# Optimization experiments

Measured on AMD Instinct MI355X. Metric: run time of the kernel, lower is better.

Reference implementation:

```python
import jax, jax.numpy as jnp
import numpy as np

B, LQ, LK, D = 32, 2048, 2048, 64


def setup_inputs() -> dict:
    key = jax.random.key(0)
    k1, k2, k3, k4 = jax.random.split(key, 4)
    querys = jax.random.normal(k1, (B, LQ, D), dtype=jnp.float32)
    keys = jax.random.normal(k2, (B, LK, D), dtype=jnp.float32)
    values = jax.random.normal(k3, (B, LK, D), dtype=jnp.float32)
    # valid lengths in [1, LK]
    valid_lens = jax.random.randint(k4, (B,), 1, LK + 1, dtype=jnp.int32)
    return {"querys": querys, "keys": keys, "values": values, "valid_lens": valid_lens}


def reference(querys, keys, values, valid_lens):
    d = querys.shape[-1]
    # [B, Lq, Lk] score matrix
    scores = jnp.einsum("bqd,bkd->bqk", querys, keys) / jnp.sqrt(jnp.asarray(d, querys.dtype))
    # masked softmax: key positions >= valid_len get -1e6 (as in d2l masked_softmax)
    key_pos = jnp.arange(scores.shape[-1], dtype=jnp.int32)  # [Lk]
    mask = key_pos[None, None, :] < valid_lens[:, None, None]  # [B, 1, Lk]
    scores = jnp.where(mask, scores, jnp.asarray(-1e6, scores.dtype))
    attn = jax.nn.softmax(scores, axis=-1)
    # dropout p=0.0 -> identity
    return jnp.einsum("bqk,bkd->bqd", attn, values)
```

## Files before the change

kernel.cpp:

```cpp
#include <hip/hip_runtime.h>
#include <hip/hip_bf16.h>
#include <math.h>


#define B_    32
#define LQ_   2048
#define LK_   2048
#define D_    64

typedef __attribute__((ext_vector_type(8)))  short bf16x8;
typedef __attribute__((ext_vector_type(4)))  float f32x4;
typedef __attribute__((ext_vector_type(16))) float f32x16;
typedef __attribute__((ext_vector_type(2)))  unsigned u32x2;

static __device__ __forceinline__ unsigned pk_bf16(float a, float b) {
    __hip_bfloat162 h = __float22bfloat162_rn(float2{a, b});
    return *(unsigned*)&h;
}

static __device__ __forceinline__ u32x2 plswap(unsigned a, unsigned b) {
    return __builtin_amdgcn_permlane32_swap(a, b, false, false);
}
static __device__ __forceinline__ float xhalf_max(float x) {
    u32x2 r = plswap(__float_as_uint(x), __float_as_uint(x));
    return fmaxf(__uint_as_float(r[0]), __uint_as_float(r[1]));
}
static __device__ __forceinline__ float xhalf_add(float x) {
    u32x2 r = plswap(__float_as_uint(x), __float_as_uint(x));
    return __uint_as_float(r[0]) + __uint_as_float(r[1]);
}

template<int NS>
__global__ __launch_bounds__(256, 2) void fa_split6_kernel(
    const float* __restrict__ Q, const float* __restrict__ K,
    const float* __restrict__ V, const int* __restrict__ vlen,
    float* __restrict__ OP, float* __restrict__ ML)
{
    __shared__ __align__(16) short Kl[2][64 * 64];
    __shared__ __align__(16) short Vt[2][64 * 64];
    __shared__ int s_b;

    const int tid  = threadIdx.x;
    const int wid  = tid >> 6;
    const int lane = tid & 63;
    const int c31  = lane & 31;
    const int h    = lane >> 5;

    constexpr int PB = 16 * NS;
    const int L    = blockIdx.x;
    const int rank = L / PB;
    const int sub  = L % PB;
    const int qb   = sub & 15;
    const int s    = sub >> 4;
    if (tid < 32) {
        const int vj = vlen[tid];
        int r = 0;
        for (int k = 0; k < 32; ++k) {
            const int vk = vlen[k];
            r += (vk > vj) || (vk == vj && k < tid);
        }
        if (r == rank) s_b = tid;
    }
    __syncthreads();
    const int b  = s_b;
    const int q0 = qb * 128 + wid * 32;
    const int vl = vlen[b];
    const int nt    = (vl + 63) >> 6;
    const int chunk = (nt + NS - 1) / NS;
    const int t0    = s * chunk;
    const int t1    = min(t0 + chunk, nt);

    const float qscale = 0.125f * 1.44269504088896340736f;

    unsigned qfrag[4][4];
#pragma unroll
    for (int ks = 0; ks < 4; ++ks) {
        const float* qp = Q + ((size_t)(b * LQ_ + q0 + c31)) * D_ + ks * 16 + h * 8;
        f32x4 t0v = *(const f32x4*)qp;
        f32x4 t1v = *(const f32x4*)(qp + 4);
#pragma unroll
        for (int jj = 0; jj < 2; ++jj) {
            qfrag[ks][jj]     = pk_bf16(t0v[2*jj] * qscale, t0v[2*jj+1] * qscale);
            qfrag[ks][jj + 2] = pk_bf16(t1v[2*jj] * qscale, t1v[2*jj+1] * qscale);
        }
    }

    f32x16 oacc[2];
#pragma unroll
    for (int dt = 0; dt < 2; ++dt)
#pragma unroll
        for (int r = 0; r < 16; ++r) oacc[dt][r] = 0.f;
    float mrun = -INFINITY, lrun = 0.f;

    const int skey = tid >> 2, skh = tid & 3;
    const int vkg = tid >> 4, vdg = tid & 15;

    const float* kgp = K + ((size_t)(b * LK_ + skey)) * D_ + skh * 16;
    const float* vgp = V + ((size_t)(b * LK_ + vkg * 4)) * D_ + vdg * 4;

    f32x4 kr[4], vr[4];
    if (t0 < t1) {
        const size_t off = (size_t)t0 * 64 * D_;
#pragma unroll
        for (int i = 0; i < 4; ++i) kr[i] = *(const f32x4*)(kgp + off + 4 * i);
#pragma unroll
        for (int i = 0; i < 4; ++i) vr[i] = *(const f32x4*)(vgp + off + (size_t)i * D_);
    }

    for (int t = t0; t < t1; ++t) {
        const int k0 = t * 64;
        const int buf = t & 1;

        {
            unsigned pk32[8];
#pragma unroll
            for (int m = 0; m < 8; ++m)
                pk32[m] = pk_bf16(kr[m >> 1][2 * (m & 1)], kr[m >> 1][2 * (m & 1) + 1]);
#pragma unroll
            for (int cch = 0; cch < 2; ++cch) {
                const int pos = (skh * 2 + cch) ^ (skey & 7);
                *(bf16x8*)&Kl[buf][skey * 64 + pos * 8] = *(bf16x8*)&pk32[4 * cch];
            }
#pragma unroll
            for (int dr = 0; dr < 4; ++dr) {
                const unsigned w0 = pk_bf16(vr[0][dr], vr[1][dr]);
                const unsigned w1 = pk_bf16(vr[2][dr], vr[3][dr]);
                const int dim = vdg * 4 + dr;
                const int pos = (vkg >> 1) ^ (dim & 7);
                uint2* dst = (uint2*)&Vt[buf][dim * 64 + pos * 8 + (vkg & 1) * 4];
                *dst = uint2{w0, w1};
            }
        }
        if (t + 1 < t1) {
            const float* kn = kgp + (size_t)(k0 + 64) * D_;
            const float* vn = vgp + (size_t)(k0 + 64) * D_;
#pragma unroll
            for (int i = 0; i < 4; ++i) kr[i] = *(const f32x4*)(kn + 4 * i);
#pragma unroll
            for (int i = 0; i < 4; ++i) vr[i] = *(const f32x4*)(vn + (size_t)i * D_);
        }
        __syncthreads();

        f32x16 st[2];
#pragma unroll
        for (int ss = 0; ss < 2; ++ss) {
#pragma unroll
            for (int r = 0; r < 16; ++r) st[ss][r] = 0.f;
#pragma unroll
            for (int ks = 0; ks < 4; ++ks) {
                const int pos = (ks * 2 + h) ^ (c31 & 7);
                bf16x8 kf = *(const bf16x8*)&Kl[buf][(ss * 32 + c31) * 64 + pos * 8];
                st[ss] = __builtin_amdgcn_mfma_f32_32x32x16_bf16(
                    kf, *(const bf16x8*)&qfrag[ks][0], st[ss], 0, 0, 0);
            }
        }

        if (k0 + 64 > vl) {
#pragma unroll
            for (int ss = 0; ss < 2; ++ss) {
                const int base = k0 + ss * 32 + 4 * h;
#pragma unroll
                for (int r = 0; r < 16; ++r) {
                    const int key = base + (r & 3) + 8 * (r >> 2);
                    if (key >= vl) st[ss][r] = -1e30f;
                }
            }
        }

        float m8[8];
#pragma unroll
        for (int r = 0; r < 8; ++r)
            m8[r] = fmaxf(fmaxf(st[0][r], st[0][r + 8]),
                          fmaxf(st[1][r], st[1][r + 8]));
#pragma unroll
        for (int o = 4; o; o >>= 1)
#pragma unroll
            for (int r = 0; r < o; ++r) m8[r] = fmaxf(m8[r], m8[r + o]);
        const float tm = xhalf_max(m8[0]);

        if (__any(tm > mrun + 8.f)) {
            const float mnew = fmaxf(mrun, tm);
            const float corr = exp2f(mrun - mnew);
            lrun *= corr;
#pragma unroll
            for (int dt = 0; dt < 2; ++dt)
#pragma unroll
                for (int r = 0; r < 16; ++r) oacc[dt][r] *= corr;
            mrun = mnew;
        }
#pragma unroll
        for (int ss = 0; ss < 2; ++ss)
#pragma unroll
            for (int r = 0; r < 16; ++r)
                st[ss][r] = exp2f(st[ss][r] - mrun);
        float s8[8];
#pragma unroll
        for (int r = 0; r < 8; ++r)
            s8[r] = (st[0][r] + st[0][r + 8]) + (st[1][r] + st[1][r + 8]);
#pragma unroll
        for (int o = 4; o; o >>= 1)
#pragma unroll
            for (int r = 0; r < o; ++r) s8[r] += s8[r + o];
        lrun += xhalf_add(s8[0]);

        unsigned pk[2][8];
#pragma unroll
        for (int ss = 0; ss < 2; ++ss)
#pragma unroll
            for (int m = 0; m < 8; ++m)
                pk[ss][m] = pk_bf16(st[ss][2 * m], st[ss][2 * m + 1]);

#pragma unroll
        for (int kq = 0; kq < 4; ++kq) {
            const int ss = kq >> 1, A4 = (kq & 1) * 4;
            u32x2 r02 = plswap(pk[ss][A4],     pk[ss][A4 + 2]);
            u32x2 r13 = plswap(pk[ss][A4 + 1], pk[ss][A4 + 3]);
            unsigned pf[4] = {r02[0], r13[0], r02[1], r13[1]};
            const bf16x8 pfr = *(const bf16x8*)&pf[0];
#pragma unroll
            for (int dt = 0; dt < 2; ++dt) {
                const int pos = (kq * 2 + h) ^ (c31 & 7);
                bf16x8 vf = *(const bf16x8*)&Vt[buf][(dt * 32 + c31) * 64 + pos * 8];
                oacc[dt] = __builtin_amdgcn_mfma_f32_32x32x16_bf16(vf, pfr, oacc[dt], 0, 0, 0);
            }
        }
    }

    const size_t row = (size_t)s * (B_ * LQ_) + b * LQ_ + q0 + c31;
    float* op = OP + row * D_;
#pragma unroll
    for (int dt = 0; dt < 2; ++dt)
#pragma unroll
        for (int g = 0; g < 4; ++g) {
            f32x4 v;
#pragma unroll
            for (int j = 0; j < 4; ++j) v[j] = oacc[dt][4 * g + j];
            *(f32x4*)(op + dt * 32 + 8 * g + 4 * h) = v;
        }
    if (h == 0)
        *(float2*)&ML[row * 2] = float2{mrun, lrun};
}

template<int NS>
__global__ __launch_bounds__(256) void fa_merge_kernel(
    const float* __restrict__ OP, const float* __restrict__ ML,
    float* __restrict__ O)
{
    const int g   = blockIdx.x * 256 + threadIdx.x;
    const int row = g >> 4;
    const int qd  = (g & 15) * 4;

    float mf = -INFINITY;
#pragma unroll
    for (int s = 0; s < NS; ++s) {
        float2 ml = *(const float2*)&ML[((size_t)s * (B_ * LQ_) + row) * 2];
        mf = fmaxf(mf, ml.x);
    }
    float den = 0.f;
    f32x4 acc = {0.f, 0.f, 0.f, 0.f};
#pragma unroll
    for (int s = 0; s < NS; ++s) {
        const size_t srow = (size_t)s * (B_ * LQ_) + row;
        float2 ml = *(const float2*)&ML[srow * 2];
        const float c = exp2f(ml.x - mf);
        den += c * ml.y;
        f32x4 v = *(const f32x4*)&OP[srow * D_ + qd];
        acc += v * c;
    }
    const float inv = 1.f / den;
    *(f32x4*)(O + (size_t)row * D_ + qd) = acc * inv;
}

__global__ __launch_bounds__(128, 2) void fa_mono_kernel(
    const float* __restrict__ Q, const float* __restrict__ K,
    const float* __restrict__ V, const int* __restrict__ vlen,
    float* __restrict__ O)
{
    __shared__ __align__(16) short Kl[2][64 * 64];
    __shared__ __align__(16) short Vt[2][64 * 64];

    const int tid  = threadIdx.x;
    const int wave = tid >> 6;
    const int lane = tid & 63;
    const int c31  = lane & 31;
    const int h    = lane >> 5;

    const int b  = blockIdx.y;
    const int q0 = blockIdx.x * 64 + wave * 32;
    const int vl = vlen[b];
    const int nt = (vl + 63) >> 6;

    const float qscale = 0.125f * 1.44269504088896340736f;

    unsigned qfrag[4][4];
#pragma unroll
    for (int ks = 0; ks < 4; ++ks) {
        const float* qp = Q + ((size_t)(b * LQ_ + q0 + c31)) * D_ + ks * 16 + h * 8;
        f32x4 t0 = *(const f32x4*)qp;
        f32x4 t1 = *(const f32x4*)(qp + 4);
#pragma unroll
        for (int jj = 0; jj < 2; ++jj) {
            qfrag[ks][jj]     = pk_bf16(t0[2*jj] * qscale, t0[2*jj+1] * qscale);
            qfrag[ks][jj + 2] = pk_bf16(t1[2*jj] * qscale, t1[2*jj+1] * qscale);
        }
    }

    f32x16 oacc[2];
#pragma unroll
    for (int dt = 0; dt < 2; ++dt)
#pragma unroll
        for (int r = 0; r < 16; ++r) oacc[dt][r] = 0.f;
    float mrun = -INFINITY, lrun = 0.f;

    const int skey = tid >> 1, skh = tid & 1;
    const int vkg = tid >> 4, vdg = tid & 15;

    const float* kgp = K + ((size_t)(b * LK_ + skey)) * D_ + skh * 32;
    const float* vgp = V + ((size_t)(b * LK_ + vkg * 8)) * D_ + vdg * 4;

    f32x4 kr[8], vr[8];
#pragma unroll
    for (int i = 0; i < 8; ++i) kr[i] = *(const f32x4*)(kgp + 4 * i);
#pragma unroll
    for (int i = 0; i < 8; ++i) vr[i] = *(const f32x4*)(vgp + (size_t)i * D_);

    for (int t = 0; t < nt; ++t) {
        const int k0 = t * 64;
        const int buf = t & 1;
        {
            unsigned pk32[16];
#pragma unroll
            for (int m = 0; m < 16; ++m)
                pk32[m] = pk_bf16(kr[m >> 1][2 * (m & 1)], kr[m >> 1][2 * (m & 1) + 1]);
#pragma unroll
            for (int cch = 0; cch < 4; ++cch) {
                const int pos = (skh * 4 + cch) ^ (skey & 7);
                *(bf16x8*)&Kl[buf][skey * 64 + pos * 8] = *(bf16x8*)&pk32[4 * cch];
            }
#pragma unroll
            for (int dr = 0; dr < 4; ++dr) {
                unsigned w[4];
#pragma unroll
                for (int p = 0; p < 4; ++p)
                    w[p] = pk_bf16(vr[2 * p][dr], vr[2 * p + 1][dr]);
                const int dim = vdg * 4 + dr;
                const int pos = vkg ^ (dim & 7);
                *(bf16x8*)&Vt[buf][dim * 64 + pos * 8] = *(bf16x8*)&w[0];
            }
        }
        if (t + 1 < nt) {
            const float* kn = kgp + (size_t)(k0 + 64) * D_;
            const float* vn = vgp + (size_t)(k0 + 64) * D_;
#pragma unroll
            for (int i = 0; i < 8; ++i) kr[i] = *(const f32x4*)(kn + 4 * i);
#pragma unroll
            for (int i = 0; i < 8; ++i) vr[i] = *(const f32x4*)(vn + (size_t)i * D_);
        }
        __syncthreads();

        f32x16 st[2];
#pragma unroll
        for (int ss = 0; ss < 2; ++ss) {
#pragma unroll
            for (int r = 0; r < 16; ++r) st[ss][r] = 0.f;
#pragma unroll
            for (int ks = 0; ks < 4; ++ks) {
                const int pos = (ks * 2 + h) ^ (c31 & 7);
                bf16x8 kf = *(const bf16x8*)&Kl[buf][(ss * 32 + c31) * 64 + pos * 8];
                st[ss] = __builtin_amdgcn_mfma_f32_32x32x16_bf16(
                    kf, *(const bf16x8*)&qfrag[ks][0], st[ss], 0, 0, 0);
            }
        }
        if (k0 + 64 > vl) {
#pragma unroll
            for (int ss = 0; ss < 2; ++ss) {
                const int base = k0 + ss * 32 + 4 * h;
#pragma unroll
                for (int r = 0; r < 16; ++r) {
                    const int key = base + (r & 3) + 8 * (r >> 2);
                    if (key >= vl) st[ss][r] = -1e30f;
                }
            }
        }
        float tm = st[0][0];
#pragma unroll
        for (int ss = 0; ss < 2; ++ss)
#pragma unroll
            for (int r = 0; r < 16; ++r) tm = fmaxf(tm, st[ss][r]);
        tm = fmaxf(tm, __shfl_xor(tm, 32));
        if (__any(tm > mrun + 8.f)) {
            const float mnew = fmaxf(mrun, tm);
            const float corr = exp2f(mrun - mnew);
            lrun *= corr;
#pragma unroll
            for (int dt = 0; dt < 2; ++dt)
#pragma unroll
                for (int r = 0; r < 16; ++r) oacc[dt][r] *= corr;
            mrun = mnew;
        }
        float rs = 0.f;
#pragma unroll
        for (int ss = 0; ss < 2; ++ss)
#pragma unroll
            for (int r = 0; r < 16; ++r) {
                const float p = exp2f(st[ss][r] - mrun);
                st[ss][r] = p;
                rs += p;
            }
        rs += __shfl_xor(rs, 32);
        lrun += rs;

        unsigned pk[2][8];
#pragma unroll
        for (int ss = 0; ss < 2; ++ss)
#pragma unroll
            for (int m = 0; m < 8; ++m)
                pk[ss][m] = pk_bf16(st[ss][2 * m], st[ss][2 * m + 1]);
#pragma unroll
        for (int kq = 0; kq < 4; ++kq) {
            const int ss = kq >> 1, A4 = (kq & 1) * 4;
            unsigned p0 = pk[ss][A4], p1 = pk[ss][A4+1], p2 = pk[ss][A4+2], p3 = pk[ss][A4+3];
            unsigned xp0 = __shfl_xor((int)p0, 32);
            unsigned xp1 = __shfl_xor((int)p1, 32);
            unsigned xp2 = __shfl_xor((int)p2, 32);
            unsigned xp3 = __shfl_xor((int)p3, 32);
            unsigned pf[4];
            pf[0] = h ? xp2 : p0;
            pf[1] = h ? xp3 : p1;
            pf[2] = h ? p2  : xp0;
            pf[3] = h ? p3  : xp1;
            const bf16x8 pfr = *(const bf16x8*)&pf[0];
#pragma unroll
            for (int dt = 0; dt < 2; ++dt) {
                const int pos = (kq * 2 + h) ^ (c31 & 7);
                bf16x8 vf = *(const bf16x8*)&Vt[buf][(dt * 32 + c31) * 64 + pos * 8];
                oacc[dt] = __builtin_amdgcn_mfma_f32_32x32x16_bf16(vf, pfr, oacc[dt], 0, 0, 0);
            }
        }
    }

    const float inv = 1.f / lrun;
    float* op = O + ((size_t)(b * LQ_ + q0 + c31)) * D_;
#pragma unroll
    for (int dt = 0; dt < 2; ++dt)
#pragma unroll
        for (int g = 0; g < 4; ++g) {
            f32x4 v;
#pragma unroll
            for (int j = 0; j < 4; ++j) v[j] = oacc[dt][4 * g + j] * inv;
            *(f32x4*)(op + dt * 32 + 8 * g + 4 * h) = v;
        }
}

extern "C" void kernel_launch(void* const* d_in, const int* in_sizes, int n_in,
                              void* d_out, int out_size, void* d_ws, size_t ws_size,
                              hipStream_t stream) {
    const float* Q    = (const float*)d_in[0];
    const float* K    = (const float*)d_in[1];
    const float* V    = (const float*)d_in[2];
    const int*   vlen = (const int*)d_in[3];
    float*       O    = (float*)d_out;

    const size_t rows = (size_t)B_ * LQ_;
    auto need = [&](int ns) { return (size_t)ns * rows * (D_ + 2) * sizeof(float); };

    int NS = 0;
    if      (d_ws && ws_size >= need(4)) NS = 4;
    else if (d_ws && ws_size >= need(2)) NS = 2;
    else if (d_ws && ws_size >= need(1)) NS = 1;

    if (NS == 0) {
        dim3 grid(LQ_ / 64, B_);
        fa_mono_kernel<<<grid, dim3(128), 0, stream>>>(Q, K, V, vlen, O);
        return;
    }

    float* OP = (float*)d_ws;
    float* ML = (float*)d_ws + (size_t)NS * rows * D_;

    const unsigned nblk = (unsigned)(16 * B_ * NS);
    switch (NS) {
        case 4: fa_split6_kernel<4><<<dim3(nblk), dim3(256), 0, stream>>>(Q, K, V, vlen, OP, ML); break;
        case 2: fa_split6_kernel<2><<<dim3(nblk), dim3(256), 0, stream>>>(Q, K, V, vlen, OP, ML); break;
        default: fa_split6_kernel<1><<<dim3(nblk), dim3(256), 0, stream>>>(Q, K, V, vlen, OP, ML); break;
    }

    dim3 g2((unsigned)((rows * (D_ / 4)) / 256));
    switch (NS) {
        case 4: fa_merge_kernel<4><<<g2, dim3(256), 0, stream>>>(OP, ML, O); break;
        case 2: fa_merge_kernel<2><<<g2, dim3(256), 0, stream>>>(OP, ML, O); break;
        default: fa_merge_kernel<1><<<g2, dim3(256), 0, stream>>>(OP, ML, O); break;
    }
}
```

Before: 152.4 us.

## Wave-level batch rank via shuffles, defer LDS stores, add MFMA priority hints

```diff
diff --git a/kernel.cpp b/kernel.cpp
--- a/kernel.cpp
+++ b/kernel.cpp
@@ -31,14 +31,13 @@
 }
 
 template<int NS>
-__global__ __launch_bounds__(256, 2) void fa_split6_kernel(
+__global__ __launch_bounds__(256, 2) void fa_split7_kernel(
     const float* __restrict__ Q, const float* __restrict__ K,
     const float* __restrict__ V, const int* __restrict__ vlen,
     float* __restrict__ OP, float* __restrict__ ML)
 {
     __shared__ __align__(16) short Kl[2][64 * 64];
     __shared__ __align__(16) short Vt[2][64 * 64];
-    __shared__ int s_b;
 
     const int tid  = threadIdx.x;
     const int wid  = tid >> 6;
@@ -52,17 +51,18 @@
     const int sub  = L % PB;
     const int qb   = sub & 15;
     const int s    = sub >> 4;
-    if (tid < 32) {
-        const int vj = vlen[tid];
+    int b;
+    {
+        const int vj = vlen[c31];
         int r = 0;
+#pragma unroll
         for (int k = 0; k < 32; ++k) {
-            const int vk = vlen[k];
-            r += (vk > vj) || (vk == vj && k < tid);
-        }
-        if (r == rank) s_b = tid;
-    }
-    __syncthreads();
-    const int b  = s_b;
+            const int vk = __shfl(vj, k);
+            r += (vk > vj) || (vk == vj && k < c31);
+        }
+        const unsigned long long match = __ballot(r == rank);
+        b = (int)(__ffsll((unsigned long long)match) - 1) & 31;
+    }
     const int q0 = qb * 128 + wid * 32;
     const int vl = vlen[b];
     const int nt    = (vl + 63) >> 6;
@@ -111,25 +111,14 @@
         const int k0 = t * 64;
         const int buf = t & 1;
 
-        {
-            unsigned pk32[8];
-#pragma unroll
-            for (int m = 0; m < 8; ++m)
-                pk32[m] = pk_bf16(kr[m >> 1][2 * (m & 1)], kr[m >> 1][2 * (m & 1) + 1]);
-#pragma unroll
-            for (int cch = 0; cch < 2; ++cch) {
-                const int pos = (skh * 2 + cch) ^ (skey & 7);
-                *(bf16x8*)&Kl[buf][skey * 64 + pos * 8] = *(bf16x8*)&pk32[4 * cch];
-            }
-#pragma unroll
-            for (int dr = 0; dr < 4; ++dr) {
-                const unsigned w0 = pk_bf16(vr[0][dr], vr[1][dr]);
-                const unsigned w1 = pk_bf16(vr[2][dr], vr[3][dr]);
-                const int dim = vdg * 4 + dr;
-                const int pos = (vkg >> 1) ^ (dim & 7);
-                uint2* dst = (uint2*)&Vt[buf][dim * 64 + pos * 8 + (vkg & 1) * 4];
-                *dst = uint2{w0, w1};
-            }
+        unsigned pk32[8], vw[8];
+#pragma unroll
+        for (int m = 0; m < 8; ++m)
+            pk32[m] = pk_bf16(kr[m >> 1][2 * (m & 1)], kr[m >> 1][2 * (m & 1) + 1]);
+#pragma unroll
+        for (int dr = 0; dr < 4; ++dr) {
+            vw[2 * dr]     = pk_bf16(vr[0][dr], vr[1][dr]);
+            vw[2 * dr + 1] = pk_bf16(vr[2][dr], vr[3][dr]);
         }
         if (t + 1 < t1) {
             const float* kn = kgp + (size_t)(k0 + 64) * D_;
@@ -139,9 +128,22 @@
 #pragma unroll
             for (int i = 0; i < 4; ++i) vr[i] = *(const f32x4*)(vn + (size_t)i * D_);
         }
+#pragma unroll
+        for (int cch = 0; cch < 2; ++cch) {
+            const int pos = (skh * 2 + cch) ^ (skey & 7);
+            *(bf16x8*)&Kl[buf][skey * 64 + pos * 8] = *(bf16x8*)&pk32[4 * cch];
+        }
+#pragma unroll
+        for (int dr = 0; dr < 4; ++dr) {
+            const int dim = vdg * 4 + dr;
+            const int pos = (vkg >> 1) ^ (dim & 7);
+            *(uint2*)&Vt[buf][dim * 64 + pos * 8 + (vkg & 1) * 4] =
+                uint2{vw[2 * dr], vw[2 * dr + 1]};
+        }
         __syncthreads();
 
         f32x16 st[2];
+        __builtin_amdgcn_s_setprio(1);
 #pragma unroll
         for (int ss = 0; ss < 2; ++ss) {
 #pragma unroll
@@ -154,6 +156,7 @@
                     kf, *(const bf16x8*)&qfrag[ks][0], st[ss], 0, 0, 0);
             }
         }
+        __builtin_amdgcn_s_setprio(0);
 
         if (k0 + 64 > vl) {
 #pragma unroll
@@ -210,6 +213,7 @@
             for (int m = 0; m < 8; ++m)
                 pk[ss][m] = pk_bf16(st[ss][2 * m], st[ss][2 * m + 1]);
 
+        __builtin_amdgcn_s_setprio(1);
 #pragma unroll
         for (int kq = 0; kq < 4; ++kq) {
             const int ss = kq >> 1, A4 = (kq & 1) * 4;
@@ -224,6 +228,7 @@
                 oacc[dt] = __builtin_amdgcn_mfma_f32_32x32x16_bf16(vf, pfr, oacc[dt], 0, 0, 0);
             }
         }
+        __builtin_amdgcn_s_setprio(0);
     }
 
     const size_t row = (size_t)s * (B_ * LQ_) + b * LQ_ + q0 + c31;
@@ -480,9 +485,9 @@
 
     const unsigned nblk = (unsigned)(16 * B_ * NS);
     switch (NS) {
-        case 4: fa_split6_kernel<4><<<dim3(nblk), dim3(256), 0, stream>>>(Q, K, V, vlen, OP, ML); break;
-        case 2: fa_split6_kernel<2><<<dim3(nblk), dim3(256), 0, stream>>>(Q, K, V, vlen, OP, ML); break;
-        default: fa_split6_kernel<1><<<dim3(nblk), dim3(256), 0, stream>>>(Q, K, V, vlen, OP, ML); break;
+        case 4: fa_split7_kernel<4><<<dim3(nblk), dim3(256), 0, stream>>>(Q, K, V, vlen, OP, ML); break;
+        case 2: fa_split7_kernel<2><<<dim3(nblk), dim3(256), 0, stream>>>(Q, K, V, vlen, OP, ML); break;
+        default: fa_split7_kernel<1><<<dim3(nblk), dim3(256), 0, stream>>>(Q, K, V, vlen, OP, ML); break;
     }
 
     dim3 g2((unsigned)((rows * (D_ / 4)) / 256));
```

Measured after the change: 155.7 us. +2.2%, slower.
